# Optimization experiments

Hardware: AMD Instinct MI355X
Metric: run time of the kernel (lower is better)

The kernel has to match this reference:

```python
import jax, jax.numpy as jnp
import numpy as np

NC = 16
NP_ = 2_000_000
Z_OFFSET = 50.0  # keep points well in front of every camera (stable 1/z)


def setup_inputs() -> dict:
    key = jax.random.key(0)
    k1, k2, k3, k4, k5 = jax.random.split(key, 5)
    pt3d = jax.random.normal(k1, (3, NP_), dtype=jnp.float32)
    R = jax.random.normal(k2, (NC, 3, 3), dtype=jnp.float32) * 0.3
    t = jax.random.normal(k3, (NC, 3), dtype=jnp.float32)
    t = t.at[:, 2].add(Z_OFFSET)
    f = jax.random.uniform(k4, (NC, 2), dtype=jnp.float32, minval=500.0, maxval=1500.0)
    c = jax.random.normal(k5, (NC, 2), dtype=jnp.float32) * 10.0
    mask = jnp.ones((NC, NP_), dtype=jnp.int32)  # full visibility (fixed output shape)
    return {"pt3d": pt3d, "R": R, "t": t, "f": f, "c": c, "mask": mask}


def reference(pt3d, R, t, f, c, mask):
    # Camera-frame points for every camera: Xc[n] = R[n] @ pt3d + t[n]  -> (Nc, 3, Np)
    Xc = jnp.einsum('nij,jp->nip', R, pt3d) + t[:, :, None]
    # Pinhole projection: (u, v) = f * (x/z, y/z) + c  -> (Nc, 2, Np)
    uv = Xc[:, :2, :] / Xc[:, 2:3, :] * f[:, :, None] + c[:, :, None]
    # Per-camera transpose to (Np, 2), then concat over cameras -> (Nc*Np, 2)
    return jnp.transpose(uv, (0, 2, 1)).reshape(-1, 2)
```

## Files before the change

kernel.cpp:

```cpp
#include <hip/hip_runtime.h>

#define NP 2000000
#define NC 16

typedef float vfloat4 __attribute__((ext_vector_type(4)));

__global__ __launch_bounds__(256) void Projection_19713899889207_kernel(
    const float* __restrict__ pt3d,
    const float* __restrict__ R,
    const float* __restrict__ t,
    const float* __restrict__ f,
    const float* __restrict__ c,
    float* __restrict__ out)
{
    const int tid = blockIdx.x * blockDim.x + threadIdx.x;
    const int p   = tid * 4;
    if (p >= NP) return;

    const vfloat4 px = *(const vfloat4*)(pt3d + 0 * NP + p);
    const vfloat4 py = *(const vfloat4*)(pt3d + 1 * NP + p);
    const vfloat4 pz = *(const vfloat4*)(pt3d + 2 * NP + p);

    float* const dst_base = out + (size_t)p * 2;

#pragma unroll 4
    for (int n = 0; n < NC; ++n) {
        const float* Rn = R + n * 9;
        const float r00 = Rn[0], r01 = Rn[1], r02 = Rn[2];
        const float r10 = Rn[3], r11 = Rn[4], r12 = Rn[5];
        const float r20 = Rn[6], r21 = Rn[7], r22 = Rn[8];
        const float t0 = t[n * 3 + 0], t1 = t[n * 3 + 1], t2 = t[n * 3 + 2];
        const float fx = f[n * 2 + 0], fy = f[n * 2 + 1];
        const float cx = c[n * 2 + 0], cy = c[n * 2 + 1];

        float u[4], v[4];
#pragma unroll
        for (int k = 0; k < 4; ++k) {
            const float x = px[k], y = py[k], z = pz[k];
            const float X = r00 * x + r01 * y + r02 * z + t0;
            const float Y = r10 * x + r11 * y + r12 * z + t1;
            const float Z = r20 * x + r21 * y + r22 * z + t2;
            const float iz = 1.0f / Z;
            u[k] = fx * X * iz + cx;
            v[k] = fy * Y * iz + cy;
        }

        vfloat4 o0, o1;
        o0.x = u[0]; o0.y = v[0]; o0.z = u[1]; o0.w = v[1];
        o1.x = u[2]; o1.y = v[2]; o1.z = u[3]; o1.w = v[3];

        vfloat4* dst = (vfloat4*)(dst_base + (size_t)n * (size_t)NP * 2);
        dst[0] = o0;
        dst[1] = o1;
    }
}

extern "C" void kernel_launch(void* const* d_in, const int* in_sizes, int n_in,
                              void* d_out, int out_size, void* d_ws, size_t ws_size,
                              hipStream_t stream) {
    const float* pt3d = (const float*)d_in[0];
    const float* R    = (const float*)d_in[1];
    const float* t    = (const float*)d_in[2];
    const float* f    = (const float*)d_in[3];
    const float* c    = (const float*)d_in[4];
    float* out = (float*)d_out;

    const int quads  = NP / 4;
    const int blocks = (quads + 255) / 256;
    Projection_19713899889207_kernel<<<blocks, 256, 0, stream>>>(pt3d, R, t, f, c, out);
}
```

Measured before the change: 344.5 us.

## Process eight points per thread with nontemporal stores and fast reciprocal

Each thread now handles eight points instead of four, loading two vec4s per coordinate and writing four vec4 outputs per camera. Output stores use nontemporal hints so the large streaming output does not pollute the caches, and the division is replaced by the hardware approximate reciprocal. The fast reciprocal gives slightly less accurate results, and the wider per-thread work halves the number of threads, which may reduce latency hiding.

```diff
diff --git a/kernel.cpp b/kernel.cpp
--- a/kernel.cpp
+++ b/kernel.cpp
@@ -14,16 +14,19 @@
     float* __restrict__ out)
 {
     const int tid = blockIdx.x * blockDim.x + threadIdx.x;
-    const int p   = tid * 4;
+    const int p   = tid * 8;
     if (p >= NP) return;
 
-    const vfloat4 px = *(const vfloat4*)(pt3d + 0 * NP + p);
-    const vfloat4 py = *(const vfloat4*)(pt3d + 1 * NP + p);
-    const vfloat4 pz = *(const vfloat4*)(pt3d + 2 * NP + p);
+    const vfloat4 px0 = *(const vfloat4*)(pt3d + 0 * NP + p);
+    const vfloat4 px1 = *(const vfloat4*)(pt3d + 0 * NP + p + 4);
+    const vfloat4 py0 = *(const vfloat4*)(pt3d + 1 * NP + p);
+    const vfloat4 py1 = *(const vfloat4*)(pt3d + 1 * NP + p + 4);
+    const vfloat4 pz0 = *(const vfloat4*)(pt3d + 2 * NP + p);
+    const vfloat4 pz1 = *(const vfloat4*)(pt3d + 2 * NP + p + 4);
 
     float* const dst_base = out + (size_t)p * 2;
 
-#pragma unroll 4
+#pragma unroll 2
     for (int n = 0; n < NC; ++n) {
         const float* Rn = R + n * 9;
         const float r00 = Rn[0], r01 = Rn[1], r02 = Rn[2];
@@ -33,25 +36,38 @@
         const float fx = f[n * 2 + 0], fy = f[n * 2 + 1];
         const float cx = c[n * 2 + 0], cy = c[n * 2 + 1];
 
-        float u[4], v[4];
+        vfloat4 o0, o1, o2, o3;
+
 #pragma unroll
         for (int k = 0; k < 4; ++k) {
-            const float x = px[k], y = py[k], z = pz[k];
+            const float x = px0[k], y = py0[k], z = pz0[k];
             const float X = r00 * x + r01 * y + r02 * z + t0;
             const float Y = r10 * x + r11 * y + r12 * z + t1;
             const float Z = r20 * x + r21 * y + r22 * z + t2;
-            const float iz = 1.0f / Z;
-            u[k] = fx * X * iz + cx;
-            v[k] = fy * Y * iz + cy;
+            const float iz = __builtin_amdgcn_rcpf(Z);
+            const float u = fx * X * iz + cx;
+            const float v = fy * Y * iz + cy;
+            if (k < 2) { o0[2 * k] = u; o0[2 * k + 1] = v; }
+            else       { o1[2 * (k - 2)] = u; o1[2 * (k - 2) + 1] = v; }
+        }
+#pragma unroll
+        for (int k = 0; k < 4; ++k) {
+            const float x = px1[k], y = py1[k], z = pz1[k];
+            const float X = r00 * x + r01 * y + r02 * z + t0;
+            const float Y = r10 * x + r11 * y + r12 * z + t1;
+            const float Z = r20 * x + r21 * y + r22 * z + t2;
+            const float iz = __builtin_amdgcn_rcpf(Z);
+            const float u = fx * X * iz + cx;
+            const float v = fy * Y * iz + cy;
+            if (k < 2) { o2[2 * k] = u; o2[2 * k + 1] = v; }
+            else       { o3[2 * (k - 2)] = u; o3[2 * (k - 2) + 1] = v; }
         }
 
-        vfloat4 o0, o1;
-        o0.x = u[0]; o0.y = v[0]; o0.z = u[1]; o0.w = v[1];
-        o1.x = u[2]; o1.y = v[2]; o1.z = u[3]; o1.w = v[3];
-
         vfloat4* dst = (vfloat4*)(dst_base + (size_t)n * (size_t)NP * 2);
-        dst[0] = o0;
-        dst[1] = o1;
+        __builtin_nontemporal_store(o0, dst + 0);
+        __builtin_nontemporal_store(o1, dst + 1);
+        __builtin_nontemporal_store(o2, dst + 2);
+        __builtin_nontemporal_store(o3, dst + 3);
     }
 }
 
@@ -65,7 +81,7 @@
     const float* c    = (const float*)d_in[4];
     float* out = (float*)d_out;
 
-    const int quads  = NP / 4;
-    const int blocks = (quads + 255) / 256;
+    const int octs   = NP / 8;
+    const int blocks = (octs + 255) / 256;
     Projection_19713899889207_kernel<<<blocks, 256, 0, stream>>>(pt3d, R, t, f, c, out);
 }
```

Result: slower. 615.3 us (+78.6%).
